# Kernel optimization log

Hardware: AMD Instinct MI355X
Metric: run time of the kernel (lower is better)

Reference implementation:

```python
import jax, jax.numpy as jnp
import numpy as np

N, M, H, K, CIN, COUT, P = 50000, 50000, 32, 15, 64, 128, 3
KP_EXTENT = 0.072
RADIUS = 0.06


def setup_inputs() -> dict:
    key = jax.random.key(0)
    ks = jax.random.split(key, 7)
    q_pts = jax.random.uniform(ks[0], (N, P), dtype=jnp.float32) * 0.05
    s_pts = jax.random.uniform(ks[1], (M, P), dtype=jnp.float32) * 0.05
    neighb_inds = jax.random.randint(ks[2], (N, H), 0, M, dtype=jnp.int64)
    x = jax.random.normal(ks[3], (M, CIN), dtype=jnp.float32)
    # kernel points inside sphere of radius RADIUS (stand-in for load_kernels)
    kernel_points = jax.random.normal(ks[4], (K, P), dtype=jnp.float32) * (0.5 * RADIUS)
    stddev = np.sqrt(1.0 / (K * COUT)).astype(np.float32)
    weights = jax.random.normal(ks[5], (K, CIN, COUT), dtype=jnp.float32) * stddev
    bias = jnp.zeros((COUT,), dtype=jnp.float32)
    return {"q_pts": q_pts, "s_pts": s_pts, "neighb_inds": neighb_inds,
            "x": x, "kernel_points": kernel_points, "weights": weights, "bias": bias}


def reference(q_pts, s_pts, neighb_inds, x, kernel_points, weights, bias):
    # pad support points with a far-away point and features with a zero row
    s_pad = jnp.concatenate([s_pts, jnp.full((1, s_pts.shape[1]), 1e6, s_pts.dtype)], axis=0)
    x_pad = jnp.concatenate([x, jnp.zeros((1, x.shape[1]), x.dtype)], axis=0)
    # gather neighbor coords/features: [N, H, P], [N, H, CIN]
    neighbors = s_pad[neighb_inds] - q_pts[:, None, :]
    neighb_x = x_pad[neighb_inds]
    # distances to kernel points: [N, H, K]
    diff = neighbors[:, :, None, :] - kernel_points  # [N, H, K, P]
    sq_d = jnp.sum(diff * diff, axis=-1)
    all_weights = jax.nn.relu(1.0 - jnp.sqrt(sq_d) / KP_EXTENT)  # linear influence
    # aggregate: [N, K, CIN] then apply per-kernel-point weights and sum over K
    weighted_features = jnp.einsum('nhk,nhc->nkc', all_weights, neighb_x)
    out = jnp.einsum('nkc,kco->no', weighted_features, weights) + bias  # [N, COUT]
    return out
```

## Files before the change

### kernel.cpp

```cpp
#include <hip/hip_runtime.h>


#define NPTS   50000
#define NPAD   50048
#define HNB    32
#define KPTS   15
#define CING   64
#define COUTG  128
#define KDIM   960
#define MSUP   50000
#define INV_EXT 13.888889f

#define X2BF_BLKS 1563
#define WT_BLKS   15
#define TWP       72

typedef __attribute__((ext_vector_type(8))) short bf16x8;
typedef __attribute__((ext_vector_type(8))) unsigned short u16x8;
typedef __attribute__((ext_vector_type(4))) float f32x4;

static __device__ __forceinline__ unsigned short f2bf(float f) {
    unsigned int u = __float_as_uint(f);
    u += 0x7FFFu + ((u >> 16) & 1u);
    return (unsigned short)(u >> 16);
}

static __device__ __forceinline__ void gload_lds16(const unsigned short* g,
                                                   unsigned short* l) {
    __builtin_amdgcn_global_load_lds(
        (const __attribute__((address_space(1))) void*)g,
        (__attribute__((address_space(3))) void*)l, 16, 0, 0);
}

__global__ __launch_bounds__(256) void kpconv_prep(const float* __restrict__ x,
                                                   unsigned short* __restrict__ xb,
                                                   const float* __restrict__ wgt,
                                                   unsigned short* __restrict__ Wt) {
    __shared__ unsigned short tw[128 * TWP];
    const int tid = threadIdx.x;
    if (blockIdx.x < X2BF_BLKS) {
        int i = (blockIdx.x * 256 + tid) * 8;
        if (i >= MSUP * CING) return;
        float4 a = *(const float4*)(x + i);
        float4 b = *(const float4*)(x + i + 4);
        u16x8 o;
        o[0] = f2bf(a.x); o[1] = f2bf(a.y); o[2] = f2bf(a.z); o[3] = f2bf(a.w);
        o[4] = f2bf(b.x); o[5] = f2bf(b.y); o[6] = f2bf(b.z); o[7] = f2bf(b.w);
        *(u16x8*)(xb + i) = o;
        return;
    }
    const int kc0 = (blockIdx.x - X2BF_BLKS) * 64;
#pragma unroll
    for (int it = 0; it < 32; ++it) {
        int idx = it * 256 + tid;
        int kcl = idx >> 7, o = idx & 127;
        tw[o * TWP + kcl] = f2bf(wgt[(size_t)(kc0 + kcl) * COUTG + o]);
    }
    __syncthreads();
#pragma unroll
    for (int it = 0; it < 4; ++it) {
        int idx = it * 256 + tid;
        int o = idx >> 3, c16 = idx & 7;
        uint4 v = *(const uint4*)&tw[o * TWP + c16 * 8];
        *(uint4*)&Wt[(size_t)o * KDIM + kc0 + c16 * 8] = v;
    }
}

__global__ __launch_bounds__(512, 4) void kpconv_agg3(
    const float* __restrict__ q_pts, const float* __restrict__ s_pts,
    const int* __restrict__ inds, const unsigned short* __restrict__ xb,
    const float* __restrict__ kpts, unsigned short* __restrict__ wf)
{
    __shared__ float4 nb[8 * HNB];

    const int tid  = threadIdx.x;
    const int wav  = tid >> 6;
    const int lane = tid & 63;
    const int l15  = lane & 15;
    const int quad = lane >> 4;
    const int n    = blockIdx.x * 8 + wav;

    if (lane < HNB) {
        int m = inds[n * HNB + lane];
        float qx = q_pts[n * 3 + 0];
        float qy = q_pts[n * 3 + 1];
        float qz = q_pts[n * 3 + 2];
        nb[wav * HNB + lane] = make_float4(s_pts[m * 3 + 0] - qx,
                                           s_pts[m * 3 + 1] - qy,
                                           s_pts[m * 3 + 2] - qz,
                                           __int_as_float(m));
    }
    __syncthreads();

    const bool kvalid = (l15 < KPTS);
    const int  kidx   = kvalid ? l15 : 0;
    const float kx = kpts[kidx * 3 + 0];
    const float ky = kpts[kidx * 3 + 1];
    const float kz = kpts[kidx * 3 + 2];

    bf16x8 af;
    const unsigned short* bj[8];
#pragma unroll
    for (int j = 0; j < 8; ++j) {
        float4 v = nb[wav * HNB + quad * 8 + j];
        bj[j] = xb + (((size_t)__float_as_int(v.w)) << 6) + l15;
        float dx = v.x - kx, dy = v.y - ky, dz = v.z - kz;
        float d  = sqrtf(dx * dx + dy * dy + dz * dz);
        float w  = kvalid ? fmaxf(0.f, 1.f - d * INV_EXT) : 0.f;
        af[j] = (short)f2bf(w);
    }

    unsigned int gv[32];
#pragma unroll
    for (int j = 0; j < 8; ++j)
#pragma unroll
        for (int nt = 0; nt < 4; ++nt)
            gv[j * 4 + nt] = bj[j][nt * 16];

    f32x4 acc[4];
#pragma unroll
    for (int nt = 0; nt < 4; ++nt) acc[nt] = (f32x4){0.f, 0.f, 0.f, 0.f};

#pragma unroll
    for (int nt = 0; nt < 4; ++nt) {
        union { unsigned int u[4]; bf16x8 f; } pk;
#pragma unroll
        for (int jj = 0; jj < 4; ++jj)
            pk.u[jj] = gv[(2 * jj) * 4 + nt] | (gv[(2 * jj + 1) * 4 + nt] << 16);
        acc[nt] = __builtin_amdgcn_mfma_f32_16x16x32_bf16(pk.f, af, acc[nt], 0, 0, 0);
    }

    if (kvalid) {
        unsigned short* wp = wf + (size_t)n * KDIM + l15 * CING + quad * 4;
#pragma unroll
        for (int nt = 0; nt < 4; ++nt) {
            unsigned int lo = (unsigned)f2bf(acc[nt][0]) | ((unsigned)f2bf(acc[nt][1]) << 16);
            unsigned int hi = (unsigned)f2bf(acc[nt][2]) | ((unsigned)f2bf(acc[nt][3]) << 16);
            *(uint2*)(wp + nt * 16) = make_uint2(lo, hi);
        }
    }
}

#define GBM 64
#define GBK 64

__global__ __launch_bounds__(256) void kpconv_gemm3(
    const unsigned short* __restrict__ A,
    const unsigned short* __restrict__ Bt,
    const float* __restrict__ bias,
    float* __restrict__ out)
{
    __shared__ unsigned short As[2][GBM * GBK];
    __shared__ unsigned short Bs[2][COUTG * GBK];

    const int tid  = threadIdx.x;
    const int wave = tid >> 6;
    const int lane = tid & 63;
    const int l15  = lane & 15;
    const int quad = lane >> 4;
    const long blockM = (long)blockIdx.x * GBM;

    f32x4 acc[8];
#pragma unroll
    for (int i = 0; i < 8; ++i) acc[i] = (f32x4){0.f, 0.f, 0.f, 0.f};

    const int rloc = lane >> 3;
    const int csw  = (lane & 7) ^ rloc;

    auto STAGE = [&](int buf, int t) {
        const int kb = t * GBK;
#pragma unroll
        for (int i = 0; i < 2; ++i) {
            const int rb = wave * 16 + i * 8;
            const unsigned short* g = A + (size_t)(blockM + rb + rloc) * KDIM + kb + csw * 8;
            gload_lds16(g, &As[buf][rb * GBK]);
        }
#pragma unroll
        for (int i = 0; i < 4; ++i) {
            const int rb = wave * 32 + i * 8;
            const unsigned short* g = Bt + (size_t)(rb + rloc) * KDIM + kb + csw * 8;
            gload_lds16(g, &Bs[buf][rb * GBK]);
        }
    };

    STAGE(0, 0);
    __syncthreads();

    for (int t = 0; t < 15; ++t) {
        const int cur = t & 1;
        if (t + 1 < 15) STAGE(cur ^ 1, t + 1);
#pragma unroll
        for (int ch = 0; ch < 2; ++ch) {
            const int soff = (((ch * 4 + quad) ^ (l15 & 7)) * 8);
            bf16x8 afr = *(const bf16x8*)&As[cur][(wave * 16 + l15) * GBK + soff];
#pragma unroll
            for (int nf = 0; nf < 8; ++nf) {
                bf16x8 bfr = *(const bf16x8*)&Bs[cur][(nf * 16 + l15) * GBK + soff];
                acc[nf] = __builtin_amdgcn_mfma_f32_16x16x32_bf16(afr, bfr, acc[nf], 0, 0, 0);
            }
        }
        __syncthreads();
    }

    const long r0 = blockM + wave * 16 + quad * 4;
#pragma unroll
    for (int nf = 0; nf < 8; ++nf) {
        const int col = nf * 16 + l15;
        const float bv = bias[col];
#pragma unroll
        for (int r = 0; r < 4; ++r) {
            long row = r0 + r;
            if (row < NPTS) out[row * COUTG + col] = acc[nf][r] + bv;
        }
    }
}

extern "C" void kernel_launch(void* const* d_in, const int* in_sizes, int n_in,
                              void* d_out, int out_size, void* d_ws, size_t ws_size,
                              hipStream_t stream) {
    const float* q_pts = (const float*)d_in[0];
    const float* s_pts = (const float*)d_in[1];
    const int*   inds  = (const int*)d_in[2];
    const float* x     = (const float*)d_in[3];
    const float* kpts  = (const float*)d_in[4];
    const float* wgt   = (const float*)d_in[5];
    const float* bias  = (const float*)d_in[6];
    float* out = (float*)d_out;

    unsigned short* wfp = (unsigned short*)d_ws;
    unsigned short* xb  = wfp + (size_t)NPAD * KDIM;
    unsigned short* Wt  = xb + (size_t)MSUP * CING;

    kpconv_prep<<<X2BF_BLKS + WT_BLKS, 256, 0, stream>>>(x, xb, wgt, Wt);
    kpconv_agg3<<<NPTS / 8, 512, 0, stream>>>(q_pts, s_pts, inds, xb, kpts, wfp);
    kpconv_gemm3<<<NPAD / GBM, 256, 0, stream>>>(wfp, Wt, bias, out);
}
```

Before: 176.7 us.

## Load GEMM operands directly from global and shrink aggregation blocks

The GEMM kernel drops its double-buffered LDS staging, which used global_load_lds and barriers, and instead has each wave read A and B fragments straight from global memory into registers for 30 unrolled MFMA steps. The aggregation kernel moves from 8 to 4 waves per block with a higher occupancy hint, and gains a scheduling barrier so all gathers are issued before the MFMAs. This removes LDS traffic and synchronisation, but every wave now re-reads the whole B matrix from cache and the A loads go uncoalesced across rows.

```diff
diff --git a/kernel.cpp b/kernel.cpp
--- a/kernel.cpp
+++ b/kernel.cpp
@@ -23,13 +23,6 @@
     unsigned int u = __float_as_uint(f);
     u += 0x7FFFu + ((u >> 16) & 1u);
     return (unsigned short)(u >> 16);
-}
-
-static __device__ __forceinline__ void gload_lds16(const unsigned short* g,
-                                                   unsigned short* l) {
-    __builtin_amdgcn_global_load_lds(
-        (const __attribute__((address_space(1))) void*)g,
-        (__attribute__((address_space(3))) void*)l, 16, 0, 0);
 }
 
 __global__ __launch_bounds__(256) void kpconv_prep(const float* __restrict__ x,
@@ -66,19 +59,19 @@
     }
 }
 
-__global__ __launch_bounds__(512, 4) void kpconv_agg3(
+__global__ __launch_bounds__(256, 5) void kpconv_agg4(
     const float* __restrict__ q_pts, const float* __restrict__ s_pts,
     const int* __restrict__ inds, const unsigned short* __restrict__ xb,
     const float* __restrict__ kpts, unsigned short* __restrict__ wf)
 {
-    __shared__ float4 nb[8 * HNB];
+    __shared__ float4 nb[4 * HNB];
 
     const int tid  = threadIdx.x;
     const int wav  = tid >> 6;
     const int lane = tid & 63;
     const int l15  = lane & 15;
     const int quad = lane >> 4;
-    const int n    = blockIdx.x * 8 + wav;
+    const int n    = blockIdx.x * 4 + wav;
 
     if (lane < HNB) {
         int m = inds[n * HNB + lane];
@@ -116,6 +109,7 @@
 #pragma unroll
         for (int nt = 0; nt < 4; ++nt)
             gv[j * 4 + nt] = bj[j][nt * 16];
+    __builtin_amdgcn_sched_barrier(0);
 
     f32x4 acc[4];
 #pragma unroll
@@ -141,65 +135,34 @@
     }
 }
 
-#define GBM 64
-#define GBK 64
-
-__global__ __launch_bounds__(256) void kpconv_gemm3(
+__global__ __launch_bounds__(256, 4) void kpconv_gemm4(
     const unsigned short* __restrict__ A,
     const unsigned short* __restrict__ Bt,
     const float* __restrict__ bias,
     float* __restrict__ out)
 {
-    __shared__ unsigned short As[2][GBM * GBK];
-    __shared__ unsigned short Bs[2][COUTG * GBK];
-
     const int tid  = threadIdx.x;
     const int wave = tid >> 6;
     const int lane = tid & 63;
     const int l15  = lane & 15;
     const int quad = lane >> 4;
-    const long blockM = (long)blockIdx.x * GBM;
+    const long blockM = (long)blockIdx.x * 64;
+
+    const unsigned short* ap = A + (size_t)(blockM + wave * 16 + l15) * KDIM + quad * 8;
+    const unsigned short* bp = Bt + (size_t)l15 * KDIM + quad * 8;
 
     f32x4 acc[8];
 #pragma unroll
     for (int i = 0; i < 8; ++i) acc[i] = (f32x4){0.f, 0.f, 0.f, 0.f};
 
-    const int rloc = lane >> 3;
-    const int csw  = (lane & 7) ^ rloc;
-
-    auto STAGE = [&](int buf, int t) {
-        const int kb = t * GBK;
-#pragma unroll
-        for (int i = 0; i < 2; ++i) {
-            const int rb = wave * 16 + i * 8;
-            const unsigned short* g = A + (size_t)(blockM + rb + rloc) * KDIM + kb + csw * 8;
-            gload_lds16(g, &As[buf][rb * GBK]);
+#pragma unroll
+    for (int s = 0; s < 30; ++s) {
+        bf16x8 afr = *(const bf16x8*)(ap + s * 32);
+#pragma unroll
+        for (int nf = 0; nf < 8; ++nf) {
+            bf16x8 bfr = *(const bf16x8*)(bp + (size_t)nf * 16 * KDIM + s * 32);
+            acc[nf] = __builtin_amdgcn_mfma_f32_16x16x32_bf16(afr, bfr, acc[nf], 0, 0, 0);
         }
-#pragma unroll
-        for (int i = 0; i < 4; ++i) {
-            const int rb = wave * 32 + i * 8;
-            const unsigned short* g = Bt + (size_t)(rb + rloc) * KDIM + kb + csw * 8;
-            gload_lds16(g, &Bs[buf][rb * GBK]);
-        }
-    };
-
-    STAGE(0, 0);
-    __syncthreads();
-
-    for (int t = 0; t < 15; ++t) {
-        const int cur = t & 1;
-        if (t + 1 < 15) STAGE(cur ^ 1, t + 1);
-#pragma unroll
-        for (int ch = 0; ch < 2; ++ch) {
-            const int soff = (((ch * 4 + quad) ^ (l15 & 7)) * 8);
-            bf16x8 afr = *(const bf16x8*)&As[cur][(wave * 16 + l15) * GBK + soff];
-#pragma unroll
-            for (int nf = 0; nf < 8; ++nf) {
-                bf16x8 bfr = *(const bf16x8*)&Bs[cur][(nf * 16 + l15) * GBK + soff];
-                acc[nf] = __builtin_amdgcn_mfma_f32_16x16x32_bf16(afr, bfr, acc[nf], 0, 0, 0);
-            }
-        }
-        __syncthreads();
     }
 
     const long r0 = blockM + wave * 16 + quad * 4;
@@ -232,6 +195,6 @@
     unsigned short* Wt  = xb + (size_t)MSUP * CING;
 
     kpconv_prep<<<X2BF_BLKS + WT_BLKS, 256, 0, stream>>>(x, xb, wgt, Wt);
-    kpconv_agg3<<<NPTS / 8, 512, 0, stream>>>(q_pts, s_pts, inds, xb, kpts, wfp);
-    kpconv_gemm3<<<NPAD / GBM, 256, 0, stream>>>(wfp, Wt, bias, out);
-}
+    kpconv_agg4<<<NPTS / 4, 256, 0, stream>>>(q_pts, s_pts, inds, xb, kpts, wfp);
+    kpconv_gemm4<<<NPAD / 64, 256, 0, stream>>>(wfp, Wt, bias, out);
+}
```

Measured after the change: 254.6 us. 1.44x slower.
